# Kernel optimization log

Hardware: AMD Instinct MI355X
Metric: run time of the kernel (lower is better)

## Reference

```python
import jax, jax.numpy as jnp
import numpy as np

S, HID = 2048, 4096
H, KV, D = 32, 8, 128
EPS = 1e-6
THETA = 10000.0


def setup_inputs() -> dict:
    key = jax.random.key(0)
    k0, k1, k2 = jax.random.split(key, 3)
    return {
        "positions": jnp.arange(S, dtype=jnp.int32),
        "hidden_states": jax.random.normal(k0, (S, HID), jnp.float32),
        "w_qkv": jax.random.normal(k1, ((H + 2 * KV) * D, HID), jnp.float32) * 0.02,
        "w_o": jax.random.normal(k2, (HID, H * D), jnp.float32) * 0.02,
        "gq": jnp.ones((D,), jnp.float32),
        "gk": jnp.ones((D,), jnp.float32),
    }


def _rmsnorm(x, g):
    # per-head RMSNorm over last dim (head_dim)
    return x * jax.lax.rsqrt(jnp.mean(x * x, axis=-1, keepdims=True) + EPS) * g


def _rope(x, positions):
    # NeoX-style rotary embedding, rotary_dim == head_dim
    half = D // 2
    inv_freq = 1.0 / (THETA ** (jnp.arange(half, dtype=jnp.float32) * 2.0 / D))
    freqs = positions.astype(jnp.float32)[:, None] * inv_freq  # [S, half]
    cos = jnp.cos(freqs)[:, None, :]  # [S, 1, half]
    sin = jnp.sin(freqs)[:, None, :]
    x1, x2 = x[..., :half], x[..., half:]
    return jnp.concatenate([x1 * cos - x2 * sin, x2 * cos + x1 * sin], axis=-1)


def reference(positions, hidden_states, w_qkv, w_o, gq, gk):
    qkv = hidden_states @ w_qkv.T  # [S, (H+2KV)*D]
    q = qkv[:, : H * D].reshape(S, H, D)
    k = qkv[:, H * D : (H + KV) * D].reshape(S, KV, D)
    v = qkv[:, (H + KV) * D :].reshape(S, KV, D)

    q = _rmsnorm(q, gq)
    k = _rmsnorm(k, gk)
    q = _rope(q, positions)
    k = _rope(k, positions)

    rep = H // KV
    kf = jnp.repeat(k, rep, axis=1)  # [S, H, D]
    vf = jnp.repeat(v, rep, axis=1)

    scale = D ** -0.5
    scores = jnp.einsum("qhd,khd->hqk", q, kf) * scale  # [H, S, S]
    causal = jnp.tril(jnp.ones((S, S), dtype=bool))
    scores = jnp.where(causal[None], scores, jnp.finfo(scores.dtype).min)
    attn = jax.nn.softmax(scores, axis=-1)
    ctx = jnp.einsum("hqk,khd->qhd", attn, vf).reshape(S, H * D)
    return ctx @ w_o.T  # [S, HID]
```

## Files before the change

kernel.cpp:

```cpp
#include <hip/hip_runtime.h>
#include <hip/hip_bf16.h>

#define S_LEN 2048
#define HID   4096
#define NH    32
#define NKV   8
#define DH    128
#define NQKV  ((NH + 2*NKV) * DH)

typedef __attribute__((ext_vector_type(8))) short s16x8;
typedef __attribute__((ext_vector_type(4))) short s16x4;
typedef __attribute__((ext_vector_type(4))) float f32x4;

__device__ __forceinline__ short f2bf(float x) {
    union { __hip_bfloat16 b; short s; } u;
    u.b = __float2bfloat16(x);
    return u.s;
}
__device__ __forceinline__ float bf2f(short s) {
    union { unsigned int u; float f; } v;
    v.u = ((unsigned int)(unsigned short)s) << 16;
    return v.f;
}

__device__ __forceinline__ void gload16(const void* g, void* l) {
    __builtin_amdgcn_global_load_lds(
        (const __attribute__((address_space(1))) void*)g,
        (__attribute__((address_space(3))) void*)l,
        16, 0, 0);
}

__device__ __forceinline__ void cstore(float* p, float v) { *p = v; }
__device__ __forceinline__ void cstore(short* p, float v) { *p = f2bf(v); }

__global__ __launch_bounds__(256) void convert_hs_wqkv(
        const float* __restrict__ in1, short* __restrict__ o1, long n1,
        const float* __restrict__ in2, short* __restrict__ o2, long n2)
{
    const long total = n1 + n2;
    long i0 = ((long)blockIdx.x * blockDim.x + threadIdx.x) * 4;
    long stride = (long)gridDim.x * blockDim.x * 4;
    for (long i = i0; i < total; i += stride) {
        const float* src; short* dst; long off;
        if (i < n1) { src = in1; dst = o1; off = i; }
        else        { src = in2; dst = o2; off = i - n1; }
        float4 v = *(const float4*)(src + off);
        s16x4 o;
        o[0] = f2bf(v.x); o[1] = f2bf(v.y); o[2] = f2bf(v.z); o[3] = f2bf(v.w);
        *(s16x4*)(dst + off) = o;
    }
}

template <typename OT>
__global__ __launch_bounds__(256, 2) void gemm192(
        const short* __restrict__ A, const short* __restrict__ B,
        OT* __restrict__ C, int M, int N, int K)
{
    __shared__ char lds[81920];
    const int t = threadIdx.x;
    const int w = t >> 6, l = t & 63, g = l >> 4, q16 = l & 15;
    const int wm = w >> 1, wn = w & 1;
    const int bx = blockIdx.x, by = blockIdx.y;
    const int NT = K >> 6;

    const int srow = t >> 3;
    const int schunk = (t & 7) ^ (srow & 7);
    unsigned goffA[4], goffB[6];
#pragma unroll
    for (int i = 0; i < 4; ++i)
        goffA[i] = (unsigned)(((by * 128 + i * 32 + srow) * K) * 2 + schunk * 16);
#pragma unroll
    for (int i = 0; i < 6; ++i)
        goffB[i] = (unsigned)(((bx * 192 + i * 32 + srow) * K) * 2 + schunk * 16);
    const int dstw = w * 1024;

    auto STAGE = [&](int kt) {
        const int par = kt & 1;
        char* dA = lds + par * 16384 + dstw;
        char* dB = lds + 32768 + par * 24576 + dstw;
        const unsigned kb = (unsigned)kt * 128;
#pragma unroll
        for (int i = 0; i < 4; ++i)
            gload16((const char*)A + (goffA[i] + kb), dA + i * 4096);
#pragma unroll
        for (int i = 0; i < 6; ++i)
            gload16((const char*)B + (goffB[i] + kb), dB + i * 4096);
    };

    int aoff[4], boff[6];
#pragma unroll
    for (int mi = 0; mi < 4; ++mi) aoff[mi] = (wm * 64 + mi * 16 + q16) * 128;
#pragma unroll
    for (int ni = 0; ni < 6; ++ni) boff[ni] = (wn * 96 + ni * 16 + q16) * 128;
    const int sw0 = ((g) ^ (q16 & 7)) << 4;
    const int sw1 = ((4 + g) ^ (q16 & 7)) << 4;

    f32x4 acc[4][6] = {};
    s16x8 aE[4][2], aO[4][2], b0E[2][2], b0O[2][2], b1[4][2];

    STAGE(0); STAGE(1);
    asm volatile("s_waitcnt vmcnt(10)" ::: "memory");
    __builtin_amdgcn_s_barrier();
    {
        const char* A0 = lds;
        const char* B0 = lds + 32768;
#pragma unroll
        for (int mi = 0; mi < 4; ++mi) {
            aE[mi][0] = *(const s16x8*)(A0 + aoff[mi] + sw0);
            aE[mi][1] = *(const s16x8*)(A0 + aoff[mi] + sw1);
        }
#pragma unroll
        for (int ni = 0; ni < 2; ++ni) {
            b0E[ni][0] = *(const s16x8*)(B0 + boff[ni] + sw0);
            b0E[ni][1] = *(const s16x8*)(B0 + boff[ni] + sw1);
        }
        asm volatile("s_waitcnt lgkmcnt(0)" ::: "memory");
        __builtin_amdgcn_sched_barrier(0);
    }

#define GB(KT, AC, AN, B0C, B0N, PAR) do {                                    \
         \
    const char* Bc_ = lds + 32768 + (PAR) * 24576;                            \
    _Pragma("unroll")                                                         \
    for (int ni = 0; ni < 4; ++ni) {                                          \
        b1[ni][0] = *(const s16x8*)(Bc_ + boff[2 + ni] + sw0);                \
        b1[ni][1] = *(const s16x8*)(Bc_ + boff[2 + ni] + sw1);                \
    }                                                                         \
    __builtin_amdgcn_sched_barrier(0);                                        \
    __builtin_amdgcn_s_setprio(1);                                            \
    _Pragma("unroll")                                                         \
    for (int mi = 0; mi < 4; ++mi)                                            \
    _Pragma("unroll")                                                         \
    for (int ni = 0; ni < 2; ++ni)                                            \
    _Pragma("unroll")                                                         \
    for (int kk = 0; kk < 2; ++kk)                                            \
        acc[mi][ni] = __builtin_amdgcn_mfma_f32_16x16x32_bf16(                \
                AC[mi][kk], B0C[ni][kk], acc[mi][ni], 0, 0, 0);               \
    __builtin_amdgcn_s_setprio(0);                                            \
                                              \
    asm volatile("s_waitcnt lgkmcnt(0)" ::: "memory");         \
    __builtin_amdgcn_sched_barrier(0);                                        \
    asm volatile("s_waitcnt vmcnt(0)" ::: "memory");        \
    __builtin_amdgcn_s_barrier();     \
                     \
    if ((KT) + 2 < NT) STAGE((KT) + 2);                                       \
    if ((KT) + 1 < NT) {                                                      \
        const char* An_ = lds + (((PAR) ^ 1) * 16384);                        \
        const char* Bn_ = lds + 32768 + ((PAR) ^ 1) * 24576;                  \
        _Pragma("unroll")                                                     \
        for (int mi = 0; mi < 4; ++mi) {                                      \
            AN[mi][0] = *(const s16x8*)(An_ + aoff[mi] + sw0);                \
            AN[mi][1] = *(const s16x8*)(An_ + aoff[mi] + sw1);                \
        }                                                                     \
        _Pragma("unroll")                                                     \
        for (int ni = 0; ni < 2; ++ni) {                                      \
            B0N[ni][0] = *(const s16x8*)(Bn_ + boff[ni] + sw0);               \
            B0N[ni][1] = *(const s16x8*)(Bn_ + boff[ni] + sw1);               \
        }                                                                     \
    }                                                                         \
    __builtin_amdgcn_sched_barrier(0);                                        \
    __builtin_amdgcn_s_setprio(1);                                            \
    _Pragma("unroll")                                                         \
    for (int mi = 0; mi < 4; ++mi)                                            \
    _Pragma("unroll")                                                         \
    for (int ni = 0; ni < 4; ++ni)                                            \
    _Pragma("unroll")                                                         \
    for (int kk = 0; kk < 2; ++kk)                                            \
        acc[mi][2 + ni] = __builtin_amdgcn_mfma_f32_16x16x32_bf16(            \
                AC[mi][kk], b1[ni][kk], acc[mi][2 + ni], 0, 0, 0);            \
    __builtin_amdgcn_s_setprio(0);                                            \
                                  \
    asm volatile("s_waitcnt lgkmcnt(0)" ::: "memory");                        \
    __builtin_amdgcn_sched_barrier(0);                                        \
} while (0)

    for (int kt = 0; kt < NT; kt += 2) {
        GB(kt,     aE, aO, b0E, b0O, 0);
        GB(kt + 1, aO, aE, b0O, b0E, 1);
    }
#undef GB

#pragma unroll
    for (int mi = 0; mi < 4; ++mi) {
        long row = (long)by * 128 + wm * 64 + mi * 16 + g * 4;
#pragma unroll
        for (int ni = 0; ni < 6; ++ni) {
            long col = (long)bx * 192 + wn * 96 + ni * 16 + q16;
            f32x4 v = acc[mi][ni];
#pragma unroll
            for (int r = 0; r < 4; ++r)
                cstore(&C[(row + r) * (long)N + col], v[r]);
        }
    }
}

template <typename OT>
__global__ __launch_bounds__(256, 2) void gemm_bt(
        const short* __restrict__ A, const short* __restrict__ B,
        OT* __restrict__ C, int M, int N, int K)
{
    __shared__ char lds[65536];
    const int t = threadIdx.x;
    const int w = t >> 6, l = t & 63, g = l >> 4, q16 = l & 15;
    const int wm = w >> 1, wn = w & 1;
    const int bx = blockIdx.x, by = blockIdx.y;
    const int NT = K >> 6;

    const int srow = t >> 3;
    const int schunk = (t & 7) ^ (srow & 7);
    unsigned goffA[4], goffB[4];
#pragma unroll
    for (int i = 0; i < 4; ++i) {
        goffA[i] = (unsigned)(((by * 128 + i * 32 + srow) * K) * 2 + schunk * 16);
        goffB[i] = (unsigned)(((bx * 128 + i * 32 + srow) * K) * 2 + schunk * 16);
    }
    const int dstw = w * 1024;

    auto STAGE = [&](int kt) {
        const int par = kt & 1;
        char* dA = lds + par * 16384 + dstw;
        char* dB = lds + 32768 + par * 16384 + dstw;
        const unsigned kb = (unsigned)kt * 128;
#pragma unroll
        for (int i = 0; i < 4; ++i) {
            gload16((const char*)A + (goffA[i] + kb), dA + i * 4096);
            gload16((const char*)B + (goffB[i] + kb), dB + i * 4096);
        }
    };

    int aoff[4], boff[4];
#pragma unroll
    for (int i = 0; i < 4; ++i) {
        aoff[i] = (wm * 64 + i * 16 + q16) * 128;
        boff[i] = (wn * 64 + i * 16 + q16) * 128;
    }
    const int sw0 = ((g) ^ (q16 & 7)) << 4;
    const int sw1 = ((4 + g) ^ (q16 & 7)) << 4;

    f32x4 acc[4][4] = {};
    s16x8 aE[4][2], aO[4][2], bf[4][2];

    STAGE(0); STAGE(1);
    asm volatile("s_waitcnt vmcnt(8)" ::: "memory");
    __builtin_amdgcn_s_barrier();
    {
        const char* A0 = lds;
#pragma unroll
        for (int mi = 0; mi < 4; ++mi) {
            aE[mi][0] = *(const s16x8*)(A0 + aoff[mi] + sw0);
            aE[mi][1] = *(const s16x8*)(A0 + aoff[mi] + sw1);
        }
    }

#define GB(KT, AC, AN, PAR) do {                                              \
    const char* Bs_ = lds + 32768 + (PAR) * 16384;                            \
    _Pragma("unroll")                                                         \
    for (int ni = 0; ni < 4; ++ni) {                                          \
        bf[ni][0] = *(const s16x8*)(Bs_ + boff[ni] + sw0);                    \
        bf[ni][1] = *(const s16x8*)(Bs_ + boff[ni] + sw1);                    \
    }                                                                         \
    asm volatile("s_waitcnt lgkmcnt(4)" ::: "memory");      \
    __builtin_amdgcn_sched_barrier(0);                                        \
    __builtin_amdgcn_s_setprio(1);                                            \
    _Pragma("unroll")                                                         \
    for (int mi = 0; mi < 4; ++mi)                                            \
    _Pragma("unroll")                                                         \
    for (int ni = 0; ni < 2; ++ni)                                            \
    _Pragma("unroll")                                                         \
    for (int kk = 0; kk < 2; ++kk)                                            \
        acc[mi][ni] = __builtin_amdgcn_mfma_f32_16x16x32_bf16(                \
                AC[mi][kk], bf[ni][kk], acc[mi][ni], 0, 0, 0);                \
    __builtin_amdgcn_s_setprio(0);                                            \
    asm volatile("s_waitcnt lgkmcnt(0)" ::: "memory");          \
    __builtin_amdgcn_sched_barrier(0);                                        \
    asm volatile("s_waitcnt vmcnt(0)" ::: "memory");        \
    __builtin_amdgcn_s_barrier();       \
    if ((KT) + 2 < NT) STAGE((KT) + 2);                                       \
    if ((KT) + 1 < NT) {                      \
        const char* An_ = lds + (((PAR) ^ 1) * 16384);                        \
        _Pragma("unroll")                                                     \
        for (int mi = 0; mi < 4; ++mi) {                                      \
            AN[mi][0] = *(const s16x8*)(An_ + aoff[mi] + sw0);                \
            AN[mi][1] = *(const s16x8*)(An_ + aoff[mi] + sw1);                \
        }                                                                     \
    }                                                                         \
    __builtin_amdgcn_s_setprio(1);                                            \
    _Pragma("unroll")                                                         \
    for (int mi = 0; mi < 4; ++mi)                                            \
    _Pragma("unroll")                                                         \
    for (int ni = 0; ni < 2; ++ni)                                            \
    _Pragma("unroll")                                                         \
    for (int kk = 0; kk < 2; ++kk)                                            \
        acc[mi][2 + ni] = __builtin_amdgcn_mfma_f32_16x16x32_bf16(            \
                AC[mi][kk], bf[2 + ni][kk], acc[mi][2 + ni], 0, 0, 0);        \
    __builtin_amdgcn_s_setprio(0);                                            \
} while (0)

    for (int kt = 0; kt < NT; kt += 2) {
        GB(kt,     aE, aO, 0);
        GB(kt + 1, aO, aE, 1);
    }
#undef GB

#pragma unroll
    for (int mi = 0; mi < 4; ++mi) {
        long row = (long)by * 128 + wm * 64 + mi * 16 + g * 4;
#pragma unroll
        for (int ni = 0; ni < 4; ++ni) {
            long col = (long)bx * 128 + wn * 64 + ni * 16 + q16;
            f32x4 v = acc[mi][ni];
#pragma unroll
            for (int r = 0; r < 4; ++r)
                cstore(&C[(row + r) * (long)N + col], v[r]);
        }
    }
}

__global__ __launch_bounds__(256) void post_gemm1_fused(
        const float* __restrict__ wo, short* __restrict__ wob,
        const short* __restrict__ qkvb, const int* __restrict__ pos,
        const float* __restrict__ gq, const float* __restrict__ gk,
        short* __restrict__ qo, short* __restrict__ ko,
        short* __restrict__ vt)
{
    const int bid = blockIdx.x;

    if (bid < 2048) {
        const long n = (long)HID * (NH * DH);
        long i0 = ((long)bid * 256 + threadIdx.x) * 4;
        long stride = 2048L * 256 * 4;
        for (long i = i0; i < n; i += stride) {
            float4 v = *(const float4*)(wo + i);
            s16x4 o;
            o[0] = f2bf(v.x); o[1] = f2bf(v.y); o[2] = f2bf(v.z); o[3] = f2bf(v.w);
            *(s16x4*)(wob + i) = o;
        }
        return;
    }

    if (bid < 12288) {
        const int idx = bid - 2048;
        const int s = idx / 5;
        const int slot = (idx % 5) * 8 + (threadIdx.x >> 5);
        const int p = threadIdx.x & 31, d = p * 4;

        s16x4 xv = *(const s16x4*)(qkvb + (long)s * NQKV + slot * DH + d);
        float x[4];
#pragma unroll
        for (int r = 0; r < 4; ++r) x[r] = bf2f(xv[r]);

        float ss = x[0]*x[0] + x[1]*x[1] + x[2]*x[2] + x[3]*x[3];
#pragma unroll
        for (int o = 1; o < 32; o <<= 1) ss += __shfl_xor(ss, o);
        float rms = rsqrtf(ss * (1.0f / DH) + 1e-6f);

        const bool isq = slot < NH;
        const float* gp = isq ? gq : gk;
        float y[4];
#pragma unroll
        for (int r = 0; r < 4; ++r) y[r] = x[r] * rms * gp[d + r];

        float y2[4];
#pragma unroll
        for (int r = 0; r < 4; ++r) y2[r] = __shfl_xor(y[r], 16);

        const float po = (float)pos[s];
        const int jbase = d & 63;
        s16x4 ov;
#pragma unroll
        for (int r = 0; r < 4; ++r) {
            float invf = exp2f(-(float)(jbase + r) * (13.287712379549449f / 64.0f));
            float ang = po * invf;
            float c = cosf(ang), sn = sinf(ang);
            float outv = (d < 64) ? (y[r] * c - y2[r] * sn)
                                  : (y[r] * c + y2[r] * sn);
            ov[r] = f2bf(outv);
        }
        if (isq) *(s16x4*)(qo + ((long)s * NH + slot) * DH + d) = ov;
        else     *(s16x4*)(ko + ((long)s * NKV + (slot - NH)) * DH + d) = ov;
        return;
    }

    __shared__ short tile[64][72];
    const int idx2 = bid - 12288;
    const int sb = idx2 & 31, db = (idx2 >> 5) & 1, h = idx2 >> 6;
    const int t = threadIdx.x;
#pragma unroll
    for (int i = 0; i < 2; ++i) {
        int c = i * 256 + t;
        int row = c >> 3, dc = (c & 7) * 8;
        const short* src = qkvb + (long)(sb*64 + row) * NQKV
                           + (NH + NKV + h) * DH + db*64 + dc;
        s16x8 x = *(const s16x8*)src;
#pragma unroll
        for (int jj = 0; jj < 8; ++jj) tile[row][dc + jj] = x[jj];
    }
    __syncthreads();
#pragma unroll
    for (int i = 0; i < 2; ++i) {
        int c = i * 256 + t;
        int dr = c >> 3, sc = (c & 7) * 8;
        s16x8 y;
#pragma unroll
        for (int jj = 0; jj < 8; ++jj) y[jj] = tile[sc + jj][dr];
        short* dst = vt + (long)(h*DH + db*64 + dr) * S_LEN + sb*64 + sc;
        *(s16x8*)dst = y;
    }
}

__device__ __forceinline__ void stage_kv(const char* kgB, const char* vgB,
                                         int kt, int t, char* kd, char* vd)
{
    const int w = t >> 6;
#pragma unroll
    for (int ci = 0; ci < 4; ++ci) {
        int c = ci * 256 + t;
        int row = c >> 4, col16 = c & 15;
        const char* gk = kgB + (long)(kt*64 + row) * (NKV*DH*2)
                         + ((col16*16) ^ ((row & 7) << 4));
        gload16(gk, kd + ci*4096 + w*1024);
        int rowv = c >> 3, scol8 = c & 7;
        const char* gv = vgB + (long)rowv * (S_LEN*2) + kt*128
                         + ((scol8*16) ^ ((rowv & 7) << 4));
        gload16(gv, vd + ci*4096 + w*1024);
    }
}

__global__ __launch_bounds__(256, 2) void attn_kernel(
        const short* __restrict__ qg, const short* __restrict__ kg,
        const short* __restrict__ vtg, short* __restrict__ ctx)
{
    const int bx = blockIdx.x;
    const int h  = bx & 31;
    const int slot = bx >> 5;
    const int qb = (slot < 8) ? slot : 23 - slot;
    const int kvh = h >> 2;
    const int t = threadIdx.x, w = t >> 6, l = t & 63, g = l >> 4, q16 = l & 15;

    __shared__ char Kl[2][16384];
    __shared__ char Vl[2][16384];
    __shared__ short Pl[4][32 * 64];

    const float scale = 0.08838834764831845f;
    const char* kgB = (const char*)kg + (long)kvh * DH * 2;
    const char* vgB = (const char*)vtg + (long)kvh * DH * (long)S_LEN * 2;

    const int nt = 2 * qb + 2;
    int qrow[2];
    qrow[0] = qb*128 + w*32 + q16;
    qrow[1] = qrow[0] + 16;

    s16x8 qf[2][4];
#pragma unroll
    for (int s = 0; s < 2; ++s) {
        const short* qptr = qg + ((long)qrow[s] * NH + h) * DH;
#pragma unroll
        for (int dk = 0; dk < 4; ++dk)
            qf[s][dk] = *(const s16x8*)(qptr + dk*32 + g*8);
    }

    f32x4 oacc[2][8] = {};
    float m_run[2] = {-1e30f, -1e30f}, l_run[2] = {0.f, 0.f};

    stage_kv(kgB, vgB, 0, t, Kl[0], Vl[0]);
    __syncthreads();

    for (int kt = 0; kt < nt; ++kt) {
        const int b = kt & 1;
        if (kt + 1 < nt)
            stage_kv(kgB, vgB, kt + 1, t, Kl[b ^ 1], Vl[b ^ 1]);
        const char* kb = Kl[b];
        const char* vbb = Vl[b];

        f32x4 sacc[2][4] = {};
        __builtin_amdgcn_s_setprio(1);
#pragma unroll
        for (int m = 0; m < 4; ++m) {
            int kvr = m*16 + q16;
            s16x8 af[4];
#pragma unroll
            for (int dk = 0; dk < 4; ++dk) {
                int byte = (kvr*256 + (dk*32 + g*8)*2) ^ ((kvr & 7) << 4);
                af[dk] = *(const s16x8*)(kb + byte);
            }
#pragma unroll
            for (int s = 0; s < 2; ++s)
#pragma unroll
                for (int dk = 0; dk < 4; ++dk)
                    sacc[s][m] = __builtin_amdgcn_mfma_f32_16x16x32_bf16(
                            af[dk], qf[s][dk], sacc[s][m], 0,0,0);
        }
        __builtin_amdgcn_s_setprio(0);

        const bool diag = (kt >= 2*qb);
        float mx[2];
#pragma unroll
        for (int s = 0; s < 2; ++s) {
            mx[s] = -1e30f;
#pragma unroll
            for (int m = 0; m < 4; ++m)
#pragma unroll
                for (int r = 0; r < 4; ++r) {
                    float x = sacc[s][m][r] * scale;
                    if (diag) {
                        int kv = kt*64 + m*16 + g*4 + r;
                        if (kv > qrow[s]) x = -1e30f;
                    }
                    sacc[s][m][r] = x;
                    mx[s] = fmaxf(mx[s], x);
                }
            mx[s] = fmaxf(mx[s], __shfl_xor(mx[s], 16));
            mx[s] = fmaxf(mx[s], __shfl_xor(mx[s], 32));
        }
        if (__any((mx[0] > m_run[0] + 8.f) || (mx[1] > m_run[1] + 8.f))) {
#pragma unroll
            for (int s = 0; s < 2; ++s) {
                float m_new = fmaxf(m_run[s], mx[s]);
                float corr = __expf(m_run[s] - m_new);
                l_run[s] *= corr;
                m_run[s] = m_new;
                float rf[4];
#pragma unroll
                for (int r = 0; r < 4; ++r)
                    rf[r] = __shfl(corr, (g << 4) | (g*4 + r));
#pragma unroll
                for (int nf = 0; nf < 8; ++nf)
#pragma unroll
                    for (int r = 0; r < 4; ++r) oacc[s][nf][r] *= rf[r];
            }
        }
#pragma unroll
        for (int s = 0; s < 2; ++s) {
            float psum = 0.f;
#pragma unroll
            for (int m = 0; m < 4; ++m) {
                s16x4 pk;
#pragma unroll
                for (int r = 0; r < 4; ++r) {
                    float e = __expf(sacc[s][m][r] - m_run[s]);
                    psum += e;
                    pk[r] = f2bf(e);
                }
                int byte = ((s*16 + q16)*128 + (m*16 + g*4)*2) ^ ((q16 & 7) << 4);
                *(s16x4*)((char*)&Pl[w][0] + byte) = pk;
            }
            psum += __shfl_xor(psum, 16);
            psum += __shfl_xor(psum, 32);
            l_run[s] += psum;
        }

        __builtin_amdgcn_s_setprio(1);
#pragma unroll
        for (int ks = 0; ks < 2; ++ks) {
            s16x8 pa[2];
#pragma unroll
            for (int s = 0; s < 2; ++s) {
                int pbyte = ((s*16 + q16)*128 + (ks*32 + g*8)*2) ^ ((q16 & 7) << 4);
                pa[s] = *(const s16x8*)((const char*)&Pl[w][0] + pbyte);
            }
#pragma unroll
            for (int nf = 0; nf < 8; ++nf) {
                int drow = nf*16 + q16;
                int vbyte = (drow*128 + (ks*32 + g*8)*2) ^ ((drow & 7) << 4);
                s16x8 vbf = *(const s16x8*)(vbb + vbyte);
#pragma unroll
                for (int s = 0; s < 2; ++s)
                    oacc[s][nf] = __builtin_amdgcn_mfma_f32_16x16x32_bf16(
                            pa[s], vbf, oacc[s][nf], 0,0,0);
            }
        }
        __builtin_amdgcn_s_setprio(0);
        __syncthreads();
    }

#pragma unroll
    for (int s = 0; s < 2; ++s) {
        float lr[4];
#pragma unroll
        for (int r = 0; r < 4; ++r)
            lr[r] = __shfl(l_run[s], (g << 4) | (g*4 + r));
#pragma unroll
        for (int nf = 0; nf < 8; ++nf)
#pragma unroll
            for (int r = 0; r < 4; ++r) {
                int row = qb*128 + w*32 + s*16 + g*4 + r;
                int col = h*DH + nf*16 + q16;
                float val = oacc[s][nf][r] / lr[r];
                ctx[(long)row * (NH*DH) + col] = f2bf(val);
            }
    }
}

extern "C" void kernel_launch(void* const* d_in, const int* in_sizes, int n_in,
                              void* d_out, int out_size, void* d_ws, size_t ws_size,
                              hipStream_t stream)
{
    const int*   positions = (const int*)  d_in[0];
    const float* hs        = (const float*)d_in[1];
    const float* wqkv      = (const float*)d_in[2];
    const float* wo        = (const float*)d_in[3];
    const float* gq        = (const float*)d_in[4];
    const float* gk        = (const float*)d_in[5];
    float* out = (float*)d_out;
    char* ws = (char*)d_ws;

    const size_t MB = 1ull << 20;
    short* hsb   = (short*)(ws);
    short* ctxb  = (short*)(ws);
    short* wqkvb = (short*)(ws + 16*MB);
    short* wob   = (short*)(ws + 16*MB);
    short* vtbuf = (short*)(ws + 48*MB);
    short* qkvb  = (short*)(ws + 67*MB);
    short* qbuf  = (short*)(ws + 91*MB);
    short* kbuf  = (short*)(ws + 107*MB);

    (void)in_sizes; (void)n_in; (void)out_size; (void)ws_size;

    convert_hs_wqkv<<<2048, 256, 0, stream>>>(
            hs, hsb, (long)S_LEN * HID,
            wqkv, wqkvb, (long)NQKV * HID);
    gemm192<short><<<dim3(NQKV/192, S_LEN/128), 256, 0, stream>>>(
            hsb, wqkvb, qkvb, S_LEN, NQKV, HID);
    post_gemm1_fused<<<12800, 256, 0, stream>>>(
            wo, wob, qkvb, positions, gq, gk, qbuf, kbuf, vtbuf);
    attn_kernel<<<dim3(512), 256, 0, stream>>>(qbuf, kbuf, vtbuf, ctxb);
    gemm_bt<float><<<dim3(HID/128, S_LEN/128), 256, 0, stream>>>(
            ctxb, wob, out, S_LEN, HID, HID);
}
```

Before: 299.7 us.

## Pre-pack hidden states into MFMA fragment layout and load A directly to registers

The conversion kernel now writes the bf16 hidden states in a packed layout that matches the MFMA A-fragment lane order, and splits the blocks between weight conversion and activation packing. The QKV GEMM then reads A fragments straight from global memory into registers, skipping the LDS staging for A. This shrinks LDS from 80KB to 48KB and removes the A ds_reads. In exchange, the A global loads now have to be covered by the pipeline, and the vmcnt waits were reworked for that. Each A tile is re-read from global/L2 by every column block instead of being shared through LDS.

New measurement: 309.2 us. 3.2% more time.

```diff
diff --git a/kernel.cpp b/kernel.cpp
--- a/kernel.cpp
+++ b/kernel.cpp
@@ -34,29 +34,42 @@
 __device__ __forceinline__ void cstore(short* p, float v) { *p = f2bf(v); }
 
 __global__ __launch_bounds__(256) void convert_hs_wqkv(
-        const float* __restrict__ in1, short* __restrict__ o1, long n1,
-        const float* __restrict__ in2, short* __restrict__ o2, long n2)
+        const float* __restrict__ hs, short* __restrict__ hsp,
+        const float* __restrict__ wq, short* __restrict__ wqb)
 {
-    const long total = n1 + n2;
-    long i0 = ((long)blockIdx.x * blockDim.x + threadIdx.x) * 4;
-    long stride = (long)gridDim.x * blockDim.x * 4;
-    for (long i = i0; i < total; i += stride) {
-        const float* src; short* dst; long off;
-        if (i < n1) { src = in1; dst = o1; off = i; }
-        else        { src = in2; dst = o2; off = i - n1; }
-        float4 v = *(const float4*)(src + off);
-        s16x4 o;
-        o[0] = f2bf(v.x); o[1] = f2bf(v.y); o[2] = f2bf(v.z); o[3] = f2bf(v.w);
-        *(s16x4*)(dst + off) = o;
+    const int bid = blockIdx.x;
+    if (bid < 1792) {
+        const long n = (long)NQKV * HID;
+        long i0 = ((long)bid * 256 + threadIdx.x) * 4;
+        long stride = 1792L * 256 * 4;
+        for (long i = i0; i < n; i += stride) {
+            float4 v = *(const float4*)(wq + i);
+            s16x4 o;
+            o[0] = f2bf(v.x); o[1] = f2bf(v.y); o[2] = f2bf(v.z); o[3] = f2bf(v.w);
+            *(s16x4*)(wqb + i) = o;
+        }
+        return;
+    }
+    const int nchunk = S_LEN * (HID / 8);
+    for (int c = (bid - 1792) * 256 + threadIdx.x; c < nchunk; c += 256 * 256) {
+        int row = c >> 9, k0 = (c & 511) << 3;
+        const float4* p = (const float4*)(hs + (long)row * HID + k0);
+        float4 v0 = p[0], v1 = p[1];
+        s16x8 o;
+        o[0] = f2bf(v0.x); o[1] = f2bf(v0.y); o[2] = f2bf(v0.z); o[3] = f2bf(v0.w);
+        o[4] = f2bf(v1.x); o[5] = f2bf(v1.y); o[6] = f2bf(v1.z); o[7] = f2bf(v1.w);
+        int lane = (row & 15) + (((k0 >> 3) & 3) << 4);
+        long off = (((long)(row >> 4) * 128 + (k0 >> 5)) * 64 + lane) * 8;
+        *(s16x8*)(hsp + off) = o;
     }
 }
 
 template <typename OT>
 __global__ __launch_bounds__(256, 2) void gemm192(
-        const short* __restrict__ A, const short* __restrict__ B,
+        const short* __restrict__ Ap, const short* __restrict__ B,
         OT* __restrict__ C, int M, int N, int K)
 {
-    __shared__ char lds[81920];
+    __shared__ char lds[49152];
     const int t = threadIdx.x;
     const int w = t >> 6, l = t & 63, g = l >> 4, q16 = l & 15;
     const int wm = w >> 1, wn = w & 1;
@@ -65,31 +78,26 @@
 
     const int srow = t >> 3;
     const int schunk = (t & 7) ^ (srow & 7);
-    unsigned goffA[4], goffB[6];
-#pragma unroll
-    for (int i = 0; i < 4; ++i)
-        goffA[i] = (unsigned)(((by * 128 + i * 32 + srow) * K) * 2 + schunk * 16);
+    unsigned goffB[6];
 #pragma unroll
     for (int i = 0; i < 6; ++i)
         goffB[i] = (unsigned)(((bx * 192 + i * 32 + srow) * K) * 2 + schunk * 16);
     const int dstw = w * 1024;
 
     auto STAGE = [&](int kt) {
-        const int par = kt & 1;
-        char* dA = lds + par * 16384 + dstw;
-        char* dB = lds + 32768 + par * 24576 + dstw;
+        char* dB = lds + (kt & 1) * 24576 + dstw;
         const unsigned kb = (unsigned)kt * 128;
-#pragma unroll
-        for (int i = 0; i < 4; ++i)
-            gload16((const char*)A + (goffA[i] + kb), dA + i * 4096);
 #pragma unroll
         for (int i = 0; i < 6; ++i)
             gload16((const char*)B + (goffB[i] + kb), dB + i * 4096);
     };
 
-    int aoff[4], boff[6];
-#pragma unroll
-    for (int mi = 0; mi < 4; ++mi) aoff[mi] = (wm * 64 + mi * 16 + q16) * 128;
+    unsigned aBase[4];
+#pragma unroll
+    for (int mi = 0; mi < 4; ++mi)
+        aBase[mi] = ((unsigned)((by * 8 + wm * 4 + mi) * 128) * 64 + (unsigned)l) * 16;
+
+    int boff[6];
 #pragma unroll
     for (int ni = 0; ni < 6; ++ni) boff[ni] = (wn * 96 + ni * 16 + q16) * 128;
     const int sw0 = ((g) ^ (q16 & 7)) << 4;
@@ -98,17 +106,19 @@
     f32x4 acc[4][6] = {};
     s16x8 aE[4][2], aO[4][2], b0E[2][2], b0O[2][2], b1[4][2];
 
-    STAGE(0); STAGE(1);
-    asm volatile("s_waitcnt vmcnt(10)" ::: "memory");
+    STAGE(0);
+    __builtin_amdgcn_sched_barrier(0);
+#pragma unroll
+    for (int mi = 0; mi < 4; ++mi)
+#pragma unroll
+        for (int kk = 0; kk < 2; ++kk)
+            aE[mi][kk] = *(const s16x8*)((const char*)Ap + aBase[mi] + kk * 1024);
+    __builtin_amdgcn_sched_barrier(0);
+    STAGE(1);
+    asm volatile("s_waitcnt vmcnt(6)" ::: "memory");
     __builtin_amdgcn_s_barrier();
     {
-        const char* A0 = lds;
-        const char* B0 = lds + 32768;
-#pragma unroll
-        for (int mi = 0; mi < 4; ++mi) {
-            aE[mi][0] = *(const s16x8*)(A0 + aoff[mi] + sw0);
-            aE[mi][1] = *(const s16x8*)(A0 + aoff[mi] + sw1);
-        }
+        const char* B0 = lds;
 #pragma unroll
         for (int ni = 0; ni < 2; ++ni) {
             b0E[ni][0] = *(const s16x8*)(B0 + boff[ni] + sw0);
@@ -119,8 +129,8 @@
     }
 
 #define GB(KT, AC, AN, B0C, B0N, PAR) do {                                    \
-         \
-    const char* Bc_ = lds + 32768 + (PAR) * 24576;                            \
+                    \
+    const char* Bc_ = lds + (PAR) * 24576;                                    \
     _Pragma("unroll")                                                         \
     for (int ni = 0; ni < 4; ++ni) {                                          \
         b1[ni][0] = *(const s16x8*)(Bc_ + boff[2 + ni] + sw0);                \
@@ -137,21 +147,24 @@
         acc[mi][ni] = __builtin_amdgcn_mfma_f32_16x16x32_bf16(                \
                 AC[mi][kk], B0C[ni][kk], acc[mi][ni], 0, 0, 0);               \
     __builtin_amdgcn_s_setprio(0);                                            \
-                                              \
-    asm volatile("s_waitcnt lgkmcnt(0)" ::: "memory");         \
-    __builtin_amdgcn_sched_barrier(0);                                        \
-    asm volatile("s_waitcnt vmcnt(0)" ::: "memory");        \
-    __builtin_amdgcn_s_barrier();     \
-                     \
+               \
+    asm volatile("s_waitcnt lgkmcnt(0)" ::: "memory");                        \
+    __builtin_amdgcn_sched_barrier(0);                                        \
+    asm volatile("s_waitcnt vmcnt(0)" ::: "memory");                          \
+    __builtin_amdgcn_s_barrier();                                             \
+         \
+    if ((KT) + 1 < NT) {                                                      \
+        _Pragma("unroll")                                                     \
+        for (int mi = 0; mi < 4; ++mi)                                        \
+        _Pragma("unroll")                                                     \
+        for (int kk = 0; kk < 2; ++kk)                                        \
+            AN[mi][kk] = *(const s16x8*)((const char*)Ap + aBase[mi]          \
+                    + (((KT) + 1) * 2 + kk) * 1024);                          \
+    }                                                                         \
+    __builtin_amdgcn_sched_barrier(0);                                        \
     if ((KT) + 2 < NT) STAGE((KT) + 2);                                       \
     if ((KT) + 1 < NT) {                                                      \
-        const char* An_ = lds + (((PAR) ^ 1) * 16384);                        \
-        const char* Bn_ = lds + 32768 + ((PAR) ^ 1) * 24576;                  \
-        _Pragma("unroll")                                                     \
-        for (int mi = 0; mi < 4; ++mi) {                                      \
-            AN[mi][0] = *(const s16x8*)(An_ + aoff[mi] + sw0);                \
-            AN[mi][1] = *(const s16x8*)(An_ + aoff[mi] + sw1);                \
-        }                                                                     \
+        const char* Bn_ = lds + ((PAR) ^ 1) * 24576;                          \
         _Pragma("unroll")                                                     \
         for (int ni = 0; ni < 2; ++ni) {                                      \
             B0N[ni][0] = *(const s16x8*)(Bn_ + boff[ni] + sw0);               \
@@ -159,6 +172,7 @@
         }                                                                     \
     }                                                                         \
     __builtin_amdgcn_sched_barrier(0);                                        \
+                                             \
     __builtin_amdgcn_s_setprio(1);                                            \
     _Pragma("unroll")                                                         \
     for (int mi = 0; mi < 4; ++mi)                                            \
@@ -169,8 +183,11 @@
         acc[mi][2 + ni] = __builtin_amdgcn_mfma_f32_16x16x32_bf16(            \
                 AC[mi][kk], b1[ni][kk], acc[mi][2 + ni], 0, 0, 0);            \
     __builtin_amdgcn_s_setprio(0);                                            \
-                                  \
+         \
     asm volatile("s_waitcnt lgkmcnt(0)" ::: "memory");                        \
+    __builtin_amdgcn_sched_barrier(0);                                        \
+    if ((KT) + 2 < NT) asm volatile("s_waitcnt vmcnt(6)" ::: "memory");       \
+    else               asm volatile("s_waitcnt vmcnt(0)" ::: "memory");       \
     __builtin_amdgcn_sched_barrier(0);                                        \
 } while (0)
 
@@ -616,9 +633,7 @@
 
     (void)in_sizes; (void)n_in; (void)out_size; (void)ws_size;
 
-    convert_hs_wqkv<<<2048, 256, 0, stream>>>(
-            hs, hsb, (long)S_LEN * HID,
-            wqkv, wqkvb, (long)NQKV * HID);
+    convert_hs_wqkv<<<2048, 256, 0, stream>>>(hs, hsb, wqkv, wqkvb);
     gemm192<short><<<dim3(NQKV/192, S_LEN/128), 256, 0, stream>>>(
             hsb, wqkvb, qkvb, S_LEN, NQKV, HID);
     post_gemm1_fused<<<12800, 256, 0, stream>>>(
```
